# Kernel tuning notes

Measured on AMD Instinct MI355X. Metric: run time of the kernel, lower is better.

## Reference

```python
import jax, jax.numpy as jnp
import numpy as np
from jax import lax

NB_ITERS = 10
HS = 3        # nb_kerhalfsize
HS_LIF = 3    # nb_kerhalfsize_LIF
DN = ('NCDHW', 'OIDHW', 'NCDHW')


def std_kernel(sigma, halfsize):
    # sigma: (C,1,1,1) -> normalized Gaussian kernel (C,1,k,k,k)
    r = jnp.arange(-halfsize, halfsize + 1, dtype=jnp.float32)
    x, y, z = jnp.meshgrid(r, r, r, indexing='ij')  # (k,k,k)
    d2 = x ** 2 + y ** 2 + z ** 2
    sig2 = sigma.reshape(-1, 1, 1, 1) ** 2          # (C,1,1,1)
    ker = jnp.exp(-d2[None] / (2.0 * sig2))         # (C,k,k,k)
    ker = ker / (ker.sum(axis=(1, 2, 3), keepdims=True) + 1e-15)
    return ker[:, None]                              # (C,1,k,k,k)


def dconv(x, ker, halfsize):
    # depthwise (grouped, groups=C) 3D conv with 'same' zero padding
    C = x.shape[1]
    pad = [(halfsize, halfsize)] * 3
    return lax.conv_general_dilated(x, ker, window_strides=(1, 1, 1),
                                    padding=pad, feature_group_count=C,
                                    dimension_numbers=DN)


def setup_inputs() -> dict:
    key = jax.random.key(0)
    k1, k2 = jax.random.split(key)
    C = 4
    shape = (1, C, 96, 96, 96)
    o = jax.random.normal(k1, shape, dtype=jnp.float32)
    I = jax.random.uniform(k2, (1, 1, 96, 96, 96), dtype=jnp.float32)
    sigma2 = jnp.ones((C, 1, 1, 1), dtype=jnp.float32)
    sigma3 = jnp.ones((C, 1, 1, 1), dtype=jnp.float32)
    eta = jnp.ones((1,), dtype=jnp.float32)
    lam = jnp.ones((1,), dtype=jnp.float32) * 5.0
    mu = jnp.ones((1,), dtype=jnp.float32) * 5.0
    return {'o': o, 'I': I, 'sigma2': sigma2, 'sigma3': sigma3,
            'eta': eta, 'lam': lam, 'mu': mu}


def reference(o, I, sigma2, sigma3, eta, lam, mu):
    u = jax.nn.softmax(o / eta, axis=1)
    ker = std_kernel(sigma2, HS)
    ker_lif = std_kernel(sigma3, HS_LIF)
    # conv of the all-ones tensor is loop-invariant (boundary normalization)
    conv_ones = dconv(jnp.ones_like(u), ker_lif, HS_LIF)
    I2 = I ** 2
    for _ in range(NB_ITERS):
        uI = u * I
        C1 = dconv(uI, ker_lif, HS_LIF)
        C2 = dconv(u, ker_lif, HS_LIF)
        Cn = (C1 + 1e-6) / (C2 + 1e-6)
        Lif = (dconv(Cn ** 2, ker_lif, HS_LIF)
               - 2.0 * I * dconv(Cn, ker_lif, HS_LIF)
               + I2 * conv_ones)
        q = dconv(1.0 - 2.0 * u, ker, HS)
        u = jax.nn.softmax((o - mu * Lif - lam * q) / eta, axis=1)
    return u
```

## Files before the change

kernel.cpp:

```cpp
#include <hip/hip_runtime.h>
#include <math.h>

#define PLANE  9216
#define PLANE4 2304
#define VOL    884736
#define VOL4   221184
#define NC     4
#define K      7
#define HSR    3
#define SEGZ   8
#define NSEGZ  12

#define YT     16
#define YTH    22
#define TPBYX  192
#define LINW   100
#define MIDW   108
#define NF4    528

__device__ __forceinline__ float4 f4zero() { return make_float4(0.f, 0.f, 0.f, 0.f); }
__device__ __forceinline__ float4 f4fma(float t, float4 a, float4 s) {
    s.x = fmaf(t, a.x, s.x); s.y = fmaf(t, a.y, s.y);
    s.z = fmaf(t, a.z, s.z); s.w = fmaf(t, a.w, s.w);
    return s;
}
__device__ __forceinline__ float4 f4fmasq(float t, float4 a, float4 s) {
    s.x = fmaf(t, a.x * a.x, s.x); s.y = fmaf(t, a.y * a.y, s.y);
    s.z = fmaf(t, a.z * a.z, s.z); s.w = fmaf(t, a.w * a.w, s.w);
    return s;
}
__device__ __forceinline__ float4 f4mul(float4 a, float4 b) {
    return make_float4(a.x * b.x, a.y * b.y, a.z * b.z, a.w * b.w);
}

__global__ void tables_kernel(const float* __restrict__ sigma2,
                              const float* __restrict__ sigma3,
                              float* __restrict__ taps2, float* __restrict__ taps3,
                              float* __restrict__ B2, float* __restrict__ B3)
{
    int t = threadIdx.x;
    if (t < 2 * NC) {
        int c = t % NC;
        const float* sig = (t < NC) ? sigma2 : sigma3;
        float* taps = (t < NC) ? taps2 : taps3;
        float sv = sig[c];
        float s2 = sv * sv;
        float w[K];
        float sum = 0.f;
        for (int j = 0; j < K; j++) {
            float d = (float)(j - HSR);
            w[j] = expf(-d * d / (2.f * s2));
            sum += w[j];
        }
        float inv = 1.f / sum;
        for (int j = 0; j < K; j++) taps[c * K + j] = w[j] * inv;
    }
    __syncthreads();
    for (int i = t; i < NC * 96; i += blockDim.x) {
        int c = i / 96, p = i % 96;
        float s2v = 0.f, s3v = 0.f;
        for (int j = 0; j < K; j++) {
            int q = p + j - HSR;
            if (q >= 0 && q < 96) { s2v += taps2[c * K + j]; s3v += taps3[c * K + j]; }
        }
        B2[i] = s2v;
        B3[i] = s3v;
    }
}

__global__ __launch_bounds__(256) void softmax0_kernel(const float* __restrict__ o,
                                                       const float* __restrict__ eta,
                                                       float* __restrict__ u)
{
    int i = blockIdx.x * 256 + threadIdx.x;
    const float4* O = (const float4*)o;
    float4* U = (float4*)u;
    float inv_eta = 1.f / eta[0];
    float4 a0 = O[i], a1 = O[i + VOL4], a2 = O[i + 2 * VOL4], a3 = O[i + 3 * VOL4];
#define SM_COMP(f)                                                              \
    {                                                                           \
        float b0 = a0.f * inv_eta, b1 = a1.f * inv_eta;                         \
        float b2 = a2.f * inv_eta, b3 = a3.f * inv_eta;                         \
        float m = fmaxf(fmaxf(b0, b1), fmaxf(b2, b3));                          \
        float e0 = __expf(b0 - m), e1 = __expf(b1 - m);                         \
        float e2 = __expf(b2 - m), e3 = __expf(b3 - m);                         \
        float inv = 1.f / (e0 + e1 + e2 + e3);                                  \
        a0.f = e0 * inv; a1.f = e1 * inv; a2.f = e2 * inv; a3.f = e3 * inv;     \
    }
    SM_COMP(x) SM_COMP(y) SM_COMP(z) SM_COMP(w)
    U[i] = a0; U[i + VOL4] = a1; U[i + 2 * VOL4] = a2; U[i + 3 * VOL4] = a3;
}

__global__ __launch_bounds__(256) void pass1_z(const float* __restrict__ u,
                                               const float* __restrict__ I,
                                               const float* __restrict__ taps2,
                                               const float* __restrict__ taps3,
                                               float* __restrict__ a0, float* __restrict__ a1,
                                               float* __restrict__ a2)
{
    int p4 = blockIdx.x * 256 + threadIdx.x;
    int s  = blockIdx.y;
    int c  = blockIdx.z;
    int z0 = s * SEGZ;
    const float4* ub = (const float4*)(u + (size_t)c * VOL) + p4;
    const float4* Ib = (const float4*)I + p4;
    float t3[K], t2[K];
#pragma unroll
    for (int j = 0; j < K; j++) { t3[j] = taps3[c * K + j]; t2[j] = taps2[c * K + j]; }
    float4 wu[K], wui[K];
#pragma unroll
    for (int j = 0; j < K - 1; j++) {
        int z = z0 + j - HSR;
        float4 uv = f4zero(), iv = f4zero();
        if (z >= 0 && z < 96) { uv = ub[z * PLANE4]; iv = Ib[z * PLANE4]; }
        wu[j] = uv; wui[j] = f4mul(uv, iv);
    }
    float4* o0 = (float4*)(a0 + (size_t)c * VOL) + p4;
    float4* o1 = (float4*)(a1 + (size_t)c * VOL) + p4;
    float4* o2 = (float4*)(a2 + (size_t)c * VOL) + p4;
    for (int k = 0; k < SEGZ; k++) {
        int z = z0 + k, zl = z + HSR;
        float4 uv = f4zero(), iv = f4zero();
        if (zl < 96) { uv = ub[zl * PLANE4]; iv = Ib[zl * PLANE4]; }
        wu[K - 1] = uv; wui[K - 1] = f4mul(uv, iv);
        float4 s0 = f4zero(), s1 = f4zero(), s2 = f4zero();
#pragma unroll
        for (int j = 0; j < K; j++) {
            s0 = f4fma(t3[j], wui[j], s0);
            s1 = f4fma(t3[j], wu[j], s1);
            s2 = f4fma(t2[j], wu[j], s2);
        }
        o0[z * PLANE4] = s0;
        o1[z * PLANE4] = s1;
        o2[z * PLANE4] = s2;
#pragma unroll
        for (int j = 0; j < K - 1; j++) { wu[j] = wu[j + 1]; wui[j] = wui[j + 1]; }
    }
}

__global__ __launch_bounds__(TPBYX) void pass2_yx(const float* __restrict__ a0,
                                                  const float* __restrict__ a1,
                                                  const float* __restrict__ a2,
                                                  const float* __restrict__ taps2,
                                                  const float* __restrict__ taps3,
                                                  const float* __restrict__ B2,
                                                  float* __restrict__ Cn,
                                                  float* __restrict__ q)
{
    __shared__ float lin[3][YTH * LINW];
    __shared__ float mid[3][YT * MIDW];
    int yt = blockIdx.x, z = blockIdx.y, c = blockIdx.z;
    int y0 = yt * YT, tid = threadIdx.x;
    size_t base = (size_t)c * VOL + (size_t)z * PLANE;
    {
        const float4* g0 = (const float4*)(a0 + base);
        const float4* g1 = (const float4*)(a1 + base);
        const float4* g2 = (const float4*)(a2 + base);
#pragma unroll
        for (int i4 = tid; i4 < NF4; i4 += TPBYX) {
            int r = i4 / 24, k = i4 - r * 24;
            int gy = y0 - HSR + r;
            bool ok = (gy >= 0 && gy < 96);
            int gi = gy * 24 + k;
            float4 v0 = ok ? g0[gi] : f4zero();
            float4 v1 = ok ? g1[gi] : f4zero();
            float4 v2 = ok ? g2[gi] : f4zero();
            int li = r * LINW + k * 4;
            *(float4*)&lin[0][li] = v0;
            *(float4*)&lin[1][li] = v1;
            *(float4*)&lin[2][li] = v2;
        }
    }
    if (tid < 128) {
        int r = tid >> 3, p = tid & 7;
        int idx = r * MIDW + (p < 4 ? p : 96 + p);
        mid[0][idx] = 0.f; mid[1][idx] = 0.f; mid[2][idx] = 0.f;
    }
    float t3[K], t2[K];
#pragma unroll
    for (int j = 0; j < K; j++) { t3[j] = taps3[c * K + j]; t2[j] = taps2[c * K + j]; }
    __syncthreads();
    int r  = tid / 12;
    int xb = (tid - r * 12) * 8;
#pragma unroll
    for (int f = 0; f < 3; f++) {
        const float* tp = (f < 2) ? t3 : t2;
        float4 mA = f4zero(), mB = f4zero();
#pragma unroll
        for (int j = 0; j < K; j++) {
            const float4* lp = (const float4*)&lin[f][(r + j) * LINW + xb];
            mA = f4fma(tp[j], lp[0], mA);
            mB = f4fma(tp[j], lp[1], mB);
        }
        float4* mp = (float4*)&mid[f][r * MIDW + 4 + xb];
        mp[0] = mA; mp[1] = mB;
    }
    __syncthreads();
    float outA[8], outB[8], outC[8];
    {
        float wf[16];
#pragma unroll
        for (int f = 0; f < 3; f++) {
            const float* tp = (f < 2) ? t3 : t2;
            const float4* wp = (const float4*)&mid[f][r * MIDW + xb];
            *(float4*)&wf[0]  = wp[0];
            *(float4*)&wf[4]  = wp[1];
            *(float4*)&wf[8]  = wp[2];
            *(float4*)&wf[12] = wp[3];
            float* dst = (f == 0) ? outA : (f == 1) ? outB : outC;
#pragma unroll
            for (int k = 0; k < 8; k++) {
                float s = 0.f;
#pragma unroll
                for (int j = 0; j < K; j++) s = fmaf(tp[j], wf[k + j + 1], s);
                dst[k] = s;
            }
        }
    }
    int y = y0 + r;
    float Bz = B2[c * 96 + z];
    float By = B2[c * 96 + y];
    float Bx[8];
    {
        const float4* bx = (const float4*)&B2[c * 96 + xb];
        *(float4*)&Bx[0] = bx[0];
        *(float4*)&Bx[4] = bx[1];
    }
    float co[8], qo[8];
#pragma unroll
    for (int k = 0; k < 8; k++) {
        co[k] = (outA[k] + 1e-6f) / (outB[k] + 1e-6f);
        qo[k] = fmaf(Bz * By, Bx[k], -2.f * outC[k]);
    }
    float* cp = Cn + base + y * 96 + xb;
    float* qp = q  + base + y * 96 + xb;
    *(float4*)cp       = *(float4*)&co[0];
    *(float4*)(cp + 4) = *(float4*)&co[4];
    *(float4*)qp       = *(float4*)&qo[0];
    *(float4*)(qp + 4) = *(float4*)&qo[4];
}

__global__ __launch_bounds__(256) void pass4_z(const float* __restrict__ Cn,
                                               const float* __restrict__ taps3,
                                               float* __restrict__ b0, float* __restrict__ b1)
{
    int p4 = blockIdx.x * 256 + threadIdx.x;
    int s  = blockIdx.y;
    int c  = blockIdx.z;
    int z0 = s * SEGZ;
    const float4* ib = (const float4*)(Cn + (size_t)c * VOL) + p4;
    float t3[K];
#pragma unroll
    for (int j = 0; j < K; j++) t3[j] = taps3[c * K + j];
    float4 w[K];
#pragma unroll
    for (int j = 0; j < K - 1; j++) {
        int z = z0 + j - HSR;
        float4 v = f4zero();
        if (z >= 0 && z < 96) v = ib[z * PLANE4];
        w[j] = v;
    }
    float4* o0 = (float4*)(b0 + (size_t)c * VOL) + p4;
    float4* o1 = (float4*)(b1 + (size_t)c * VOL) + p4;
    for (int k = 0; k < SEGZ; k++) {
        int z = z0 + k, zl = z + HSR;
        float4 v = f4zero();
        if (zl < 96) v = ib[zl * PLANE4];
        w[K - 1] = v;
        float4 s0 = f4zero(), s1 = f4zero();
#pragma unroll
        for (int j = 0; j < K; j++) {
            s0 = f4fma(t3[j], w[j], s0);
            s1 = f4fmasq(t3[j], w[j], s1);
        }
        o0[z * PLANE4] = s0;
        o1[z * PLANE4] = s1;
#pragma unroll
        for (int j = 0; j < K - 1; j++) w[j] = w[j + 1];
    }
}

__global__ __launch_bounds__(TPBYX) void pass5_yx(const float* __restrict__ cz0,
                                                  const float* __restrict__ cz1,
                                                  const float* __restrict__ q,
                                                  const float* __restrict__ o,
                                                  const float* __restrict__ I,
                                                  const float* __restrict__ taps3,
                                                  const float* __restrict__ B3,
                                                  const float* __restrict__ eta,
                                                  const float* __restrict__ lam,
                                                  const float* __restrict__ mu,
                                                  float* __restrict__ argb)
{
    __shared__ float lin[2][YTH * LINW];
    __shared__ float mid[2][YT * MIDW];
    int yt = blockIdx.x, z = blockIdx.y, c = blockIdx.z;
    int y0 = yt * YT, tid = threadIdx.x;
    size_t base = (size_t)c * VOL + (size_t)z * PLANE;
    {
        const float4* g0 = (const float4*)(cz0 + base);
        const float4* g1 = (const float4*)(cz1 + base);
#pragma unroll
        for (int i4 = tid; i4 < NF4; i4 += TPBYX) {
            int r = i4 / 24, k = i4 - r * 24;
            int gy = y0 - HSR + r;
            bool ok = (gy >= 0 && gy < 96);
            int gi = gy * 24 + k;
            float4 v0 = ok ? g0[gi] : f4zero();
            float4 v1 = ok ? g1[gi] : f4zero();
            int li = r * LINW + k * 4;
            *(float4*)&lin[0][li] = v0;
            *(float4*)&lin[1][li] = v1;
        }
    }
    if (tid < 128) {
        int r = tid >> 3, p = tid & 7;
        int idx = r * MIDW + (p < 4 ? p : 96 + p);
        mid[0][idx] = 0.f; mid[1][idx] = 0.f;
    }
    float t3[K];
#pragma unroll
    for (int j = 0; j < K; j++) t3[j] = taps3[c * K + j];
    __syncthreads();
    int r  = tid / 12;
    int xb = (tid - r * 12) * 8;
#pragma unroll
    for (int f = 0; f < 2; f++) {
        float4 mA = f4zero(), mB = f4zero();
#pragma unroll
        for (int j = 0; j < K; j++) {
            const float4* lp = (const float4*)&lin[f][(r + j) * LINW + xb];
            mA = f4fma(t3[j], lp[0], mA);
            mB = f4fma(t3[j], lp[1], mB);
        }
        float4* mp = (float4*)&mid[f][r * MIDW + 4 + xb];
        mp[0] = mA; mp[1] = mB;
    }
    __syncthreads();
    float d0[8], d1[8];
    {
        float wf[16];
#pragma unroll
        for (int f = 0; f < 2; f++) {
            const float4* wp = (const float4*)&mid[f][r * MIDW + xb];
            *(float4*)&wf[0]  = wp[0];
            *(float4*)&wf[4]  = wp[1];
            *(float4*)&wf[8]  = wp[2];
            *(float4*)&wf[12] = wp[3];
            float* dst = (f == 0) ? d0 : d1;
#pragma unroll
            for (int k = 0; k < 8; k++) {
                float s = 0.f;
#pragma unroll
                for (int j = 0; j < K; j++) s = fmaf(t3[j], wf[k + j + 1], s);
                dst[k] = s;
            }
        }
    }
    int y = y0 + r;
    int v = z * PLANE + y * 96 + xb;
    float inv_eta = 1.f / eta[0];
    float lamv = lam[0], muv = mu[0];
    float Bz = B3[c * 96 + z];
    float By = B3[c * 96 + y];
    float Bx[8], Ivv[8], ov[8], qv[8];
    {
        const float4* bx = (const float4*)&B3[c * 96 + xb];
        *(float4*)&Bx[0] = bx[0]; *(float4*)&Bx[4] = bx[1];
        const float4* ip = (const float4*)&I[v];
        *(float4*)&Ivv[0] = ip[0]; *(float4*)&Ivv[4] = ip[1];
        const float4* op = (const float4*)&o[(size_t)c * VOL + v];
        *(float4*)&ov[0] = op[0]; *(float4*)&ov[4] = op[1];
        const float4* qp = (const float4*)&q[(size_t)c * VOL + v];
        *(float4*)&qv[0] = qp[0]; *(float4*)&qv[4] = qp[1];
    }
    float res[8];
#pragma unroll
    for (int k = 0; k < 8; k++) {
        float Iv = Ivv[k];
        float cones = Bz * By * Bx[k];
        float Lif = d1[k] - 2.f * Iv * d0[k] + Iv * Iv * cones;
        res[k] = (ov[k] - muv * Lif - lamv * qv[k]) * inv_eta;
    }
    float* ap = argb + base + y * 96 + xb;
    *(float4*)ap       = *(float4*)&res[0];
    *(float4*)(ap + 4) = *(float4*)&res[4];
}

__global__ __launch_bounds__(256) void pass6_softmax(const float* __restrict__ argb,
                                                     float* __restrict__ u)
{
    int i = blockIdx.x * 256 + threadIdx.x;
    const float4* A = (const float4*)argb;
    float4* U = (float4*)u;
    float4 a0 = A[i], a1 = A[i + VOL4], a2 = A[i + 2 * VOL4], a3 = A[i + 3 * VOL4];
#define SM2_COMP(f)                                                             \
    {                                                                           \
        float m = fmaxf(fmaxf(a0.f, a1.f), fmaxf(a2.f, a3.f));                  \
        float e0 = __expf(a0.f - m), e1 = __expf(a1.f - m);                     \
        float e2 = __expf(a2.f - m), e3 = __expf(a3.f - m);                     \
        float inv = 1.f / (e0 + e1 + e2 + e3);                                  \
        a0.f = e0 * inv; a1.f = e1 * inv; a2.f = e2 * inv; a3.f = e3 * inv;     \
    }
    SM2_COMP(x) SM2_COMP(y) SM2_COMP(z) SM2_COMP(w)
    U[i] = a0; U[i + VOL4] = a1; U[i + 2 * VOL4] = a2; U[i + 3 * VOL4] = a3;
}

extern "C" void kernel_launch(void* const* d_in, const int* in_sizes, int n_in,
                              void* d_out, int out_size, void* d_ws, size_t ws_size,
                              hipStream_t stream)
{
    const float* o      = (const float*)d_in[0];
    const float* I      = (const float*)d_in[1];
    const float* sigma2 = (const float*)d_in[2];
    const float* sigma3 = (const float*)d_in[3];
    const float* eta    = (const float*)d_in[4];
    const float* lam    = (const float*)d_in[5];
    const float* mu     = (const float*)d_in[6];
    float* u = (float*)d_out;

    float* wsf = (float*)d_ws;
    float* taps2 = wsf;
    float* taps3 = wsf + 32;
    float* B2    = wsf + 64;
    float* B3    = wsf + 64 + NC * 96;
    float* buf   = wsf + 1024;
    const size_t VCs = (size_t)NC * VOL;
    float* a0 = buf;
    float* a1 = buf + VCs;
    float* a2 = buf + 2 * VCs;
    float* Cn = buf + 3 * VCs;
    float* qb = buf + 4 * VCs;
    float* c0 = buf + 5 * VCs;
    float* c1 = buf + 6 * VCs;

    const dim3 gridZ(PLANE4 / 256, NSEGZ, NC);
    const dim3 gridYX(96 / YT, 96, NC);
    const int gridV4 = VOL4 / 256;

    tables_kernel<<<1, 512, 0, stream>>>(sigma2, sigma3, taps2, taps3, B2, B3);
    softmax0_kernel<<<gridV4, 256, 0, stream>>>(o, eta, u);
    for (int it = 0; it < 10; it++) {
        pass1_z<<<gridZ, 256, 0, stream>>>(u, I, taps2, taps3, a0, a1, a2);
        pass2_yx<<<gridYX, TPBYX, 0, stream>>>(a0, a1, a2, taps2, taps3, B2, Cn, qb);
        pass4_z<<<gridZ, 256, 0, stream>>>(Cn, taps3, c0, c1);
        pass5_yx<<<gridYX, TPBYX, 0, stream>>>(c0, c1, qb, o, I, taps3, B3,
                                               eta, lam, mu, a0);
        pass6_softmax<<<gridV4, 256, 0, stream>>>(a0, u);
    }
}
```

Measured before the change: 704.6 us.

## Fuse softmax into z-pass and drop separate softmax kernel per iteration

Each iteration's softmax is now folded into the first z-direction conv pass: pass1 reads the raw logits for all four channels, computes the softmax on the fly for each plane it loads, and convolves. The softmax kernel and the write and read of u are gone from the loop, and the final softmax runs once at the end. This trades a full-volume read and write per iteration for recomputing the softmax on every plane load, about 7x redundant exp work, with fewer threads (64 per block, 2 floats each). pass4 also gets retuned block and segment sizes, and pass5 now writes its logits into the Cn buffer.

After: 728.6 us. +3.4%, slower.

```diff
diff --git a/kernel.cpp b/kernel.cpp
--- a/kernel.cpp
+++ b/kernel.cpp
@@ -2,14 +2,18 @@
 #include <math.h>
 
 #define PLANE  9216
+#define PLANE2 4608
 #define PLANE4 2304
 #define VOL    884736
+#define VOL2   442368
 #define VOL4   221184
 #define NC     4
 #define K      7
 #define HSR    3
 #define SEGZ   8
 #define NSEGZ  12
+#define SEGZ4  16
+#define NSEGZ4 6
 
 #define YT     16
 #define YTH    22
@@ -29,8 +33,10 @@
     s.z = fmaf(t, a.z * a.z, s.z); s.w = fmaf(t, a.w * a.w, s.w);
     return s;
 }
-__device__ __forceinline__ float4 f4mul(float4 a, float4 b) {
-    return make_float4(a.x * b.x, a.y * b.y, a.z * b.z, a.w * b.w);
+__device__ __forceinline__ float2 f2zero() { return make_float2(0.f, 0.f); }
+__device__ __forceinline__ float2 f2fma(float t, float2 a, float2 s) {
+    s.x = fmaf(t, a.x, s.x); s.y = fmaf(t, a.y, s.y);
+    return s;
 }
 
 __global__ void tables_kernel(const float* __restrict__ sigma2,
@@ -91,51 +97,93 @@
     U[i] = a0; U[i + VOL4] = a1; U[i + 2 * VOL4] = a2; U[i + 3 * VOL4] = a3;
 }
 
-__global__ __launch_bounds__(256) void pass1_z(const float* __restrict__ u,
-                                               const float* __restrict__ I,
-                                               const float* __restrict__ taps2,
-                                               const float* __restrict__ taps3,
-                                               float* __restrict__ a0, float* __restrict__ a1,
-                                               float* __restrict__ a2)
-{
-    int p4 = blockIdx.x * 256 + threadIdx.x;
-    int s  = blockIdx.y;
-    int c  = blockIdx.z;
-    int z0 = s * SEGZ;
-    const float4* ub = (const float4*)(u + (size_t)c * VOL) + p4;
-    const float4* Ib = (const float4*)I + p4;
-    float t3[K], t2[K];
-#pragma unroll
-    for (int j = 0; j < K; j++) { t3[j] = taps3[c * K + j]; t2[j] = taps2[c * K + j]; }
-    float4 wu[K], wui[K];
-#pragma unroll
-    for (int j = 0; j < K - 1; j++) {
-        int z = z0 + j - HSR;
-        float4 uv = f4zero(), iv = f4zero();
-        if (z >= 0 && z < 96) { uv = ub[z * PLANE4]; iv = Ib[z * PLANE4]; }
-        wu[j] = uv; wui[j] = f4mul(uv, iv);
-    }
-    float4* o0 = (float4*)(a0 + (size_t)c * VOL) + p4;
-    float4* o1 = (float4*)(a1 + (size_t)c * VOL) + p4;
-    float4* o2 = (float4*)(a2 + (size_t)c * VOL) + p4;
+__global__ __launch_bounds__(64) void pass1f(const float* __restrict__ araw,
+                                             const float* __restrict__ I,
+                                             const float* __restrict__ taps2,
+                                             const float* __restrict__ taps3,
+                                             const float* __restrict__ eta,
+                                             float* __restrict__ a0, float* __restrict__ a1,
+                                             float* __restrict__ a2)
+{
+    int p2 = blockIdx.x * 64 + threadIdx.x;
+    int z0 = blockIdx.y * SEGZ;
+    float inv_eta = 1.f / eta[0];
+    float t3[NC][K], t2[NC][K];
+#pragma unroll
+    for (int c = 0; c < NC; c++)
+#pragma unroll
+        for (int j = 0; j < K; j++) { t3[c][j] = taps3[c * K + j]; t2[c][j] = taps2[c * K + j]; }
+    const float2* A  = (const float2*)araw;
+    const float2* Ip = (const float2*)I;
+    float2 uw[NC][K];
+    float2 iw[K];
+
+#define LOADPLANE(zz, dst_j)                                                     \
+    {                                                                            \
+        int z_ = (zz);                                                           \
+        if (z_ >= 0 && z_ < 96) {                                                \
+            int off = z_ * PLANE2 + p2;                                          \
+            float2 q0 = A[off];                                                  \
+            float2 q1 = A[off + VOL2];                                           \
+            float2 q2 = A[off + 2 * VOL2];                                       \
+            float2 q3 = A[off + 3 * VOL2];                                       \
+            iw[dst_j] = Ip[off];                                                 \
+            float b0, b1, b2, b3, m_, e0, e1, e2, e3, inv_;                      \
+            b0 = q0.x * inv_eta; b1 = q1.x * inv_eta;                            \
+            b2 = q2.x * inv_eta; b3 = q3.x * inv_eta;                            \
+            m_ = fmaxf(fmaxf(b0, b1), fmaxf(b2, b3));                            \
+            e0 = __expf(b0 - m_); e1 = __expf(b1 - m_);                          \
+            e2 = __expf(b2 - m_); e3 = __expf(b3 - m_);                          \
+            inv_ = 1.f / (e0 + e1 + e2 + e3);                                    \
+            uw[0][dst_j].x = e0 * inv_; uw[1][dst_j].x = e1 * inv_;              \
+            uw[2][dst_j].x = e2 * inv_; uw[3][dst_j].x = e3 * inv_;              \
+            b0 = q0.y * inv_eta; b1 = q1.y * inv_eta;                            \
+            b2 = q2.y * inv_eta; b3 = q3.y * inv_eta;                            \
+            m_ = fmaxf(fmaxf(b0, b1), fmaxf(b2, b3));                            \
+            e0 = __expf(b0 - m_); e1 = __expf(b1 - m_);                          \
+            e2 = __expf(b2 - m_); e3 = __expf(b3 - m_);                          \
+            inv_ = 1.f / (e0 + e1 + e2 + e3);                                    \
+            uw[0][dst_j].y = e0 * inv_; uw[1][dst_j].y = e1 * inv_;              \
+            uw[2][dst_j].y = e2 * inv_; uw[3][dst_j].y = e3 * inv_;              \
+        } else {                                                                 \
+            iw[dst_j] = f2zero();                                                \
+            uw[0][dst_j] = f2zero(); uw[1][dst_j] = f2zero();                    \
+            uw[2][dst_j] = f2zero(); uw[3][dst_j] = f2zero();                    \
+        }                                                                        \
+    }
+
+#pragma unroll
+    for (int j = 0; j < K - 1; j++) LOADPLANE(z0 + j - HSR, j)
+
+    float2* O0 = (float2*)a0;
+    float2* O1 = (float2*)a1;
+    float2* O2 = (float2*)a2;
     for (int k = 0; k < SEGZ; k++) {
-        int z = z0 + k, zl = z + HSR;
-        float4 uv = f4zero(), iv = f4zero();
-        if (zl < 96) { uv = ub[zl * PLANE4]; iv = Ib[zl * PLANE4]; }
-        wu[K - 1] = uv; wui[K - 1] = f4mul(uv, iv);
-        float4 s0 = f4zero(), s1 = f4zero(), s2 = f4zero();
-#pragma unroll
-        for (int j = 0; j < K; j++) {
-            s0 = f4fma(t3[j], wui[j], s0);
-            s1 = f4fma(t3[j], wu[j], s1);
-            s2 = f4fma(t2[j], wu[j], s2);
-        }
-        o0[z * PLANE4] = s0;
-        o1[z * PLANE4] = s1;
-        o2[z * PLANE4] = s2;
-#pragma unroll
-        for (int j = 0; j < K - 1; j++) { wu[j] = wu[j + 1]; wui[j] = wui[j + 1]; }
-    }
+        LOADPLANE(z0 + k + HSR, K - 1)
+        int ob = (z0 + k) * PLANE2 + p2;
+#pragma unroll
+        for (int c = 0; c < NC; c++) {
+            float2 s0 = f2zero(), s1 = f2zero(), s2 = f2zero();
+#pragma unroll
+            for (int j = 0; j < K; j++) {
+                float2 uv = uw[c][j];
+                float2 ui = make_float2(uv.x * iw[j].x, uv.y * iw[j].y);
+                s0 = f2fma(t3[c][j], ui, s0);
+                s1 = f2fma(t3[c][j], uv, s1);
+                s2 = f2fma(t2[c][j], uv, s2);
+            }
+            O0[c * VOL2 + ob] = s0;
+            O1[c * VOL2 + ob] = s1;
+            O2[c * VOL2 + ob] = s2;
+        }
+#pragma unroll
+        for (int j = 0; j < K - 1; j++) {
+            iw[j] = iw[j + 1];
+#pragma unroll
+            for (int c = 0; c < NC; c++) uw[c][j] = uw[c][j + 1];
+        }
+    }
+#undef LOADPLANE
 }
 
 __global__ __launch_bounds__(TPBYX) void pass2_yx(const float* __restrict__ a0,
@@ -240,14 +288,14 @@
     *(float4*)(qp + 4) = *(float4*)&qo[4];
 }
 
-__global__ __launch_bounds__(256) void pass4_z(const float* __restrict__ Cn,
+__global__ __launch_bounds__(128) void pass4_z(const float* __restrict__ Cn,
                                                const float* __restrict__ taps3,
                                                float* __restrict__ b0, float* __restrict__ b1)
 {
-    int p4 = blockIdx.x * 256 + threadIdx.x;
+    int p4 = blockIdx.x * 128 + threadIdx.x;
     int s  = blockIdx.y;
     int c  = blockIdx.z;
-    int z0 = s * SEGZ;
+    int z0 = s * SEGZ4;
     const float4* ib = (const float4*)(Cn + (size_t)c * VOL) + p4;
     float t3[K];
 #pragma unroll
@@ -262,7 +310,7 @@
     }
     float4* o0 = (float4*)(b0 + (size_t)c * VOL) + p4;
     float4* o1 = (float4*)(b1 + (size_t)c * VOL) + p4;
-    for (int k = 0; k < SEGZ; k++) {
+    for (int k = 0; k < SEGZ4; k++) {
         int z = z0 + k, zl = z + HSR;
         float4 v = f4zero();
         if (zl < 96) v = ib[zl * PLANE4];
@@ -287,7 +335,6 @@
                                                   const float* __restrict__ I,
                                                   const float* __restrict__ taps3,
                                                   const float* __restrict__ B3,
-                                                  const float* __restrict__ eta,
                                                   const float* __restrict__ lam,
                                                   const float* __restrict__ mu,
                                                   float* __restrict__ argb)
@@ -359,7 +406,6 @@
     }
     int y = y0 + r;
     int v = z * PLANE + y * 96 + xb;
-    float inv_eta = 1.f / eta[0];
     float lamv = lam[0], muv = mu[0];
     float Bz = B3[c * 96 + z];
     float By = B3[c * 96 + y];
@@ -380,30 +426,11 @@
         float Iv = Ivv[k];
         float cones = Bz * By * Bx[k];
         float Lif = d1[k] - 2.f * Iv * d0[k] + Iv * Iv * cones;
-        res[k] = (ov[k] - muv * Lif - lamv * qv[k]) * inv_eta;
+        res[k] = ov[k] - muv * Lif - lamv * qv[k];
     }
     float* ap = argb + base + y * 96 + xb;
     *(float4*)ap       = *(float4*)&res[0];
     *(float4*)(ap + 4) = *(float4*)&res[4];
-}
-
-__global__ __launch_bounds__(256) void pass6_softmax(const float* __restrict__ argb,
-                                                     float* __restrict__ u)
-{
-    int i = blockIdx.x * 256 + threadIdx.x;
-    const float4* A = (const float4*)argb;
-    float4* U = (float4*)u;
-    float4 a0 = A[i], a1 = A[i + VOL4], a2 = A[i + 2 * VOL4], a3 = A[i + 3 * VOL4];
-#define SM2_COMP(f)                                                             \
-    {                                                                           \
-        float m = fmaxf(fmaxf(a0.f, a1.f), fmaxf(a2.f, a3.f));                  \
-        float e0 = __expf(a0.f - m), e1 = __expf(a1.f - m);                     \
-        float e2 = __expf(a2.f - m), e3 = __expf(a3.f - m);                     \
-        float inv = 1.f / (e0 + e1 + e2 + e3);                                  \
-        a0.f = e0 * inv; a1.f = e1 * inv; a2.f = e2 * inv; a3.f = e3 * inv;     \
-    }
-    SM2_COMP(x) SM2_COMP(y) SM2_COMP(z) SM2_COMP(w)
-    U[i] = a0; U[i + VOL4] = a1; U[i + 2 * VOL4] = a2; U[i + 3 * VOL4] = a3;
 }
 
 extern "C" void kernel_launch(void* const* d_in, const int* in_sizes, int n_in,
@@ -434,18 +461,19 @@
     float* c0 = buf + 5 * VCs;
     float* c1 = buf + 6 * VCs;
 
-    const dim3 gridZ(PLANE4 / 256, NSEGZ, NC);
+    const dim3 grid1(PLANE2 / 64, NSEGZ);
     const dim3 gridYX(96 / YT, 96, NC);
+    const dim3 grid4(PLANE4 / 128, NSEGZ4, NC);
     const int gridV4 = VOL4 / 256;
 
     tables_kernel<<<1, 512, 0, stream>>>(sigma2, sigma3, taps2, taps3, B2, B3);
-    softmax0_kernel<<<gridV4, 256, 0, stream>>>(o, eta, u);
     for (int it = 0; it < 10; it++) {
-        pass1_z<<<gridZ, 256, 0, stream>>>(u, I, taps2, taps3, a0, a1, a2);
+        const float* argin = (it == 0) ? o : Cn;
+        pass1f<<<grid1, 64, 0, stream>>>(argin, I, taps2, taps3, eta, a0, a1, a2);
         pass2_yx<<<gridYX, TPBYX, 0, stream>>>(a0, a1, a2, taps2, taps3, B2, Cn, qb);
-        pass4_z<<<gridZ, 256, 0, stream>>>(Cn, taps3, c0, c1);
+        pass4_z<<<grid4, 128, 0, stream>>>(Cn, taps3, c0, c1);
         pass5_yx<<<gridYX, TPBYX, 0, stream>>>(c0, c1, qb, o, I, taps3, B3,
-                                               eta, lam, mu, a0);
-        pass6_softmax<<<gridV4, 256, 0, stream>>>(a0, u);
-    }
-}
+                                               lam, mu, Cn);
+    }
+    softmax0_kernel<<<gridV4, 256, 0, stream>>>(Cn, eta, u);
+}
```

## Move q yx-convolution into pass5 and reuse eta-scaling softmax kernel

Applied to the files above, without the earlier changes.

The yx smoothing of the q field (a2) moves from pass2 into pass5, so the intermediate q buffer is no longer written and read back each iteration. pass2 now handles only the two LIF fields, and pass5 handles three. The separate final softmax kernel is replaced by the initial softmax kernel, which applies 1/eta itself, so pass5 drops its eta multiply. pass4_z also switches to 128-thread blocks with 16-slice z segments, giving more blocks with less halo reload. The cost is heavier shared-memory use and register pressure in pass5.

Result: no change. 714.9 us (+1.5%).

```diff
diff --git a/kernel.cpp b/kernel.cpp
--- a/kernel.cpp
+++ b/kernel.cpp
@@ -10,6 +10,8 @@
 #define HSR    3
 #define SEGZ   8
 #define NSEGZ  12
+#define SEGZ4  16
+#define NSEGZ4 6
 
 #define YT     16
 #define YTH    22
@@ -68,15 +70,15 @@
     }
 }
 
-__global__ __launch_bounds__(256) void softmax0_kernel(const float* __restrict__ o,
-                                                       const float* __restrict__ eta,
-                                                       float* __restrict__ u)
+__global__ __launch_bounds__(256) void softmax_kernel(const float* __restrict__ a,
+                                                      const float* __restrict__ eta,
+                                                      float* __restrict__ u)
 {
     int i = blockIdx.x * 256 + threadIdx.x;
-    const float4* O = (const float4*)o;
+    const float4* A = (const float4*)a;
     float4* U = (float4*)u;
     float inv_eta = 1.f / eta[0];
-    float4 a0 = O[i], a1 = O[i + VOL4], a2 = O[i + 2 * VOL4], a3 = O[i + 3 * VOL4];
+    float4 a0 = A[i], a1 = A[i + VOL4], a2 = A[i + 2 * VOL4], a3 = A[i + 3 * VOL4];
 #define SM_COMP(f)                                                              \
     {                                                                           \
         float b0 = a0.f * inv_eta, b1 = a1.f * inv_eta;                         \
@@ -140,12 +142,137 @@
 
 __global__ __launch_bounds__(TPBYX) void pass2_yx(const float* __restrict__ a0,
                                                   const float* __restrict__ a1,
+                                                  const float* __restrict__ taps3,
+                                                  float* __restrict__ Cn)
+{
+    __shared__ float lin[2][YTH * LINW];
+    __shared__ float mid[2][YT * MIDW];
+    int yt = blockIdx.x, z = blockIdx.y, c = blockIdx.z;
+    int y0 = yt * YT, tid = threadIdx.x;
+    size_t base = (size_t)c * VOL + (size_t)z * PLANE;
+    {
+        const float4* g0 = (const float4*)(a0 + base);
+        const float4* g1 = (const float4*)(a1 + base);
+#pragma unroll
+        for (int i4 = tid; i4 < NF4; i4 += TPBYX) {
+            int r = i4 / 24, k = i4 - r * 24;
+            int gy = y0 - HSR + r;
+            bool ok = (gy >= 0 && gy < 96);
+            int gi = gy * 24 + k;
+            float4 v0 = ok ? g0[gi] : f4zero();
+            float4 v1 = ok ? g1[gi] : f4zero();
+            int li = r * LINW + k * 4;
+            *(float4*)&lin[0][li] = v0;
+            *(float4*)&lin[1][li] = v1;
+        }
+    }
+    if (tid < 128) {
+        int r = tid >> 3, p = tid & 7;
+        int idx = r * MIDW + (p < 4 ? p : 96 + p);
+        mid[0][idx] = 0.f; mid[1][idx] = 0.f;
+    }
+    float t3[K];
+#pragma unroll
+    for (int j = 0; j < K; j++) t3[j] = taps3[c * K + j];
+    __syncthreads();
+    int r  = tid / 12;
+    int xb = (tid - r * 12) * 8;
+#pragma unroll
+    for (int f = 0; f < 2; f++) {
+        float4 mA = f4zero(), mB = f4zero();
+#pragma unroll
+        for (int j = 0; j < K; j++) {
+            const float4* lp = (const float4*)&lin[f][(r + j) * LINW + xb];
+            mA = f4fma(t3[j], lp[0], mA);
+            mB = f4fma(t3[j], lp[1], mB);
+        }
+        float4* mp = (float4*)&mid[f][r * MIDW + 4 + xb];
+        mp[0] = mA; mp[1] = mB;
+    }
+    __syncthreads();
+    float outA[8], outB[8];
+    {
+        float wf[16];
+#pragma unroll
+        for (int f = 0; f < 2; f++) {
+            const float4* wp = (const float4*)&mid[f][r * MIDW + xb];
+            *(float4*)&wf[0]  = wp[0];
+            *(float4*)&wf[4]  = wp[1];
+            *(float4*)&wf[8]  = wp[2];
+            *(float4*)&wf[12] = wp[3];
+            float* dst = (f == 0) ? outA : outB;
+#pragma unroll
+            for (int k = 0; k < 8; k++) {
+                float s = 0.f;
+#pragma unroll
+                for (int j = 0; j < K; j++) s = fmaf(t3[j], wf[k + j + 1], s);
+                dst[k] = s;
+            }
+        }
+    }
+    int y = y0 + r;
+    float co[8];
+#pragma unroll
+    for (int k = 0; k < 8; k++)
+        co[k] = (outA[k] + 1e-6f) / (outB[k] + 1e-6f);
+    float* cp = Cn + base + y * 96 + xb;
+    *(float4*)cp       = *(float4*)&co[0];
+    *(float4*)(cp + 4) = *(float4*)&co[4];
+}
+
+__global__ __launch_bounds__(128) void pass4_z(const float* __restrict__ Cn,
+                                               const float* __restrict__ taps3,
+                                               float* __restrict__ b0, float* __restrict__ b1)
+{
+    int p4 = blockIdx.x * 128 + threadIdx.x;
+    int s  = blockIdx.y;
+    int c  = blockIdx.z;
+    int z0 = s * SEGZ4;
+    const float4* ib = (const float4*)(Cn + (size_t)c * VOL) + p4;
+    float t3[K];
+#pragma unroll
+    for (int j = 0; j < K; j++) t3[j] = taps3[c * K + j];
+    float4 w[K];
+#pragma unroll
+    for (int j = 0; j < K - 1; j++) {
+        int z = z0 + j - HSR;
+        float4 v = f4zero();
+        if (z >= 0 && z < 96) v = ib[z * PLANE4];
+        w[j] = v;
+    }
+    float4* o0 = (float4*)(b0 + (size_t)c * VOL) + p4;
+    float4* o1 = (float4*)(b1 + (size_t)c * VOL) + p4;
+    for (int k = 0; k < SEGZ4; k++) {
+        int z = z0 + k, zl = z + HSR;
+        float4 v = f4zero();
+        if (zl < 96) v = ib[zl * PLANE4];
+        w[K - 1] = v;
+        float4 s0 = f4zero(), s1 = f4zero();
+#pragma unroll
+        for (int j = 0; j < K; j++) {
+            s0 = f4fma(t3[j], w[j], s0);
+            s1 = f4fmasq(t3[j], w[j], s1);
+        }
+        o0[z * PLANE4] = s0;
+        o1[z * PLANE4] = s1;
+#pragma unroll
+        for (int j = 0; j < K - 1; j++) w[j] = w[j + 1];
+    }
+}
+
+__global__ __launch_bounds__(TPBYX) void pass5_yx(const float* __restrict__ cz0,
+                                                  const float* __restrict__ cz1,
                                                   const float* __restrict__ a2,
+                                                  const float* __restrict__ o,
+                                                  const float* __restrict__ I,
                                                   const float* __restrict__ taps2,
                                                   const float* __restrict__ taps3,
                                                   const float* __restrict__ B2,
-                                                  float* __restrict__ Cn,
-                                                  float* __restrict__ q)
+                                                  const float* __restrict__ B3,
+                                                  const float* __restrict__ eta,
+                                                  const float* __restrict__ lam,
+                                                  const float* __restrict__ mu,
+                                                  float* __restrict__ argb)
 {
     __shared__ float lin[3][YTH * LINW];
     __shared__ float mid[3][YT * MIDW];
@@ -153,8 +280,8 @@
     int y0 = yt * YT, tid = threadIdx.x;
     size_t base = (size_t)c * VOL + (size_t)z * PLANE;
     {
-        const float4* g0 = (const float4*)(a0 + base);
-        const float4* g1 = (const float4*)(a1 + base);
+        const float4* g0 = (const float4*)(cz0 + base);
+        const float4* g1 = (const float4*)(cz1 + base);
         const float4* g2 = (const float4*)(a2 + base);
 #pragma unroll
         for (int i4 = tid; i4 < NF4; i4 += TPBYX) {
@@ -196,7 +323,7 @@
         mp[0] = mA; mp[1] = mB;
     }
     __syncthreads();
-    float outA[8], outB[8], outC[8];
+    float d0[8], d1[8], s2[8];
     {
         float wf[16];
 #pragma unroll
@@ -207,152 +334,12 @@
             *(float4*)&wf[4]  = wp[1];
             *(float4*)&wf[8]  = wp[2];
             *(float4*)&wf[12] = wp[3];
-            float* dst = (f == 0) ? outA : (f == 1) ? outB : outC;
+            float* dst = (f == 0) ? d0 : (f == 1) ? d1 : s2;
 #pragma unroll
             for (int k = 0; k < 8; k++) {
                 float s = 0.f;
 #pragma unroll
                 for (int j = 0; j < K; j++) s = fmaf(tp[j], wf[k + j + 1], s);
-                dst[k] = s;
-            }
-        }
-    }
-    int y = y0 + r;
-    float Bz = B2[c * 96 + z];
-    float By = B2[c * 96 + y];
-    float Bx[8];
-    {
-        const float4* bx = (const float4*)&B2[c * 96 + xb];
-        *(float4*)&Bx[0] = bx[0];
-        *(float4*)&Bx[4] = bx[1];
-    }
-    float co[8], qo[8];
-#pragma unroll
-    for (int k = 0; k < 8; k++) {
-        co[k] = (outA[k] + 1e-6f) / (outB[k] + 1e-6f);
-        qo[k] = fmaf(Bz * By, Bx[k], -2.f * outC[k]);
-    }
-    float* cp = Cn + base + y * 96 + xb;
-    float* qp = q  + base + y * 96 + xb;
-    *(float4*)cp       = *(float4*)&co[0];
-    *(float4*)(cp + 4) = *(float4*)&co[4];
-    *(float4*)qp       = *(float4*)&qo[0];
-    *(float4*)(qp + 4) = *(float4*)&qo[4];
-}
-
-__global__ __launch_bounds__(256) void pass4_z(const float* __restrict__ Cn,
-                                               const float* __restrict__ taps3,
-                                               float* __restrict__ b0, float* __restrict__ b1)
-{
-    int p4 = blockIdx.x * 256 + threadIdx.x;
-    int s  = blockIdx.y;
-    int c  = blockIdx.z;
-    int z0 = s * SEGZ;
-    const float4* ib = (const float4*)(Cn + (size_t)c * VOL) + p4;
-    float t3[K];
-#pragma unroll
-    for (int j = 0; j < K; j++) t3[j] = taps3[c * K + j];
-    float4 w[K];
-#pragma unroll
-    for (int j = 0; j < K - 1; j++) {
-        int z = z0 + j - HSR;
-        float4 v = f4zero();
-        if (z >= 0 && z < 96) v = ib[z * PLANE4];
-        w[j] = v;
-    }
-    float4* o0 = (float4*)(b0 + (size_t)c * VOL) + p4;
-    float4* o1 = (float4*)(b1 + (size_t)c * VOL) + p4;
-    for (int k = 0; k < SEGZ; k++) {
-        int z = z0 + k, zl = z + HSR;
-        float4 v = f4zero();
-        if (zl < 96) v = ib[zl * PLANE4];
-        w[K - 1] = v;
-        float4 s0 = f4zero(), s1 = f4zero();
-#pragma unroll
-        for (int j = 0; j < K; j++) {
-            s0 = f4fma(t3[j], w[j], s0);
-            s1 = f4fmasq(t3[j], w[j], s1);
-        }
-        o0[z * PLANE4] = s0;
-        o1[z * PLANE4] = s1;
-#pragma unroll
-        for (int j = 0; j < K - 1; j++) w[j] = w[j + 1];
-    }
-}
-
-__global__ __launch_bounds__(TPBYX) void pass5_yx(const float* __restrict__ cz0,
-                                                  const float* __restrict__ cz1,
-                                                  const float* __restrict__ q,
-                                                  const float* __restrict__ o,
-                                                  const float* __restrict__ I,
-                                                  const float* __restrict__ taps3,
-                                                  const float* __restrict__ B3,
-                                                  const float* __restrict__ eta,
-                                                  const float* __restrict__ lam,
-                                                  const float* __restrict__ mu,
-                                                  float* __restrict__ argb)
-{
-    __shared__ float lin[2][YTH * LINW];
-    __shared__ float mid[2][YT * MIDW];
-    int yt = blockIdx.x, z = blockIdx.y, c = blockIdx.z;
-    int y0 = yt * YT, tid = threadIdx.x;
-    size_t base = (size_t)c * VOL + (size_t)z * PLANE;
-    {
-        const float4* g0 = (const float4*)(cz0 + base);
-        const float4* g1 = (const float4*)(cz1 + base);
-#pragma unroll
-        for (int i4 = tid; i4 < NF4; i4 += TPBYX) {
-            int r = i4 / 24, k = i4 - r * 24;
-            int gy = y0 - HSR + r;
-            bool ok = (gy >= 0 && gy < 96);
-            int gi = gy * 24 + k;
-            float4 v0 = ok ? g0[gi] : f4zero();
-            float4 v1 = ok ? g1[gi] : f4zero();
-            int li = r * LINW + k * 4;
-            *(float4*)&lin[0][li] = v0;
-            *(float4*)&lin[1][li] = v1;
-        }
-    }
-    if (tid < 128) {
-        int r = tid >> 3, p = tid & 7;
-        int idx = r * MIDW + (p < 4 ? p : 96 + p);
-        mid[0][idx] = 0.f; mid[1][idx] = 0.f;
-    }
-    float t3[K];
-#pragma unroll
-    for (int j = 0; j < K; j++) t3[j] = taps3[c * K + j];
-    __syncthreads();
-    int r  = tid / 12;
-    int xb = (tid - r * 12) * 8;
-#pragma unroll
-    for (int f = 0; f < 2; f++) {
-        float4 mA = f4zero(), mB = f4zero();
-#pragma unroll
-        for (int j = 0; j < K; j++) {
-            const float4* lp = (const float4*)&lin[f][(r + j) * LINW + xb];
-            mA = f4fma(t3[j], lp[0], mA);
-            mB = f4fma(t3[j], lp[1], mB);
-        }
-        float4* mp = (float4*)&mid[f][r * MIDW + 4 + xb];
-        mp[0] = mA; mp[1] = mB;
-    }
-    __syncthreads();
-    float d0[8], d1[8];
-    {
-        float wf[16];
-#pragma unroll
-        for (int f = 0; f < 2; f++) {
-            const float4* wp = (const float4*)&mid[f][r * MIDW + xb];
-            *(float4*)&wf[0]  = wp[0];
-            *(float4*)&wf[4]  = wp[1];
-            *(float4*)&wf[8]  = wp[2];
-            *(float4*)&wf[12] = wp[3];
-            float* dst = (f == 0) ? d0 : d1;
-#pragma unroll
-            for (int k = 0; k < 8; k++) {
-                float s = 0.f;
-#pragma unroll
-                for (int j = 0; j < K; j++) s = fmaf(t3[j], wf[k + j + 1], s);
                 dst[k] = s;
             }
         }
@@ -361,49 +348,31 @@
     int v = z * PLANE + y * 96 + xb;
     float inv_eta = 1.f / eta[0];
     float lamv = lam[0], muv = mu[0];
-    float Bz = B3[c * 96 + z];
-    float By = B3[c * 96 + y];
-    float Bx[8], Ivv[8], ov[8], qv[8];
+    float Bz3 = B3[c * 96 + z], By3 = B3[c * 96 + y];
+    float Bz2 = B2[c * 96 + z], By2 = B2[c * 96 + y];
+    float Bx3[8], Bx2[8], Ivv[8], ov[8];
     {
-        const float4* bx = (const float4*)&B3[c * 96 + xb];
-        *(float4*)&Bx[0] = bx[0]; *(float4*)&Bx[4] = bx[1];
+        const float4* bx3 = (const float4*)&B3[c * 96 + xb];
+        *(float4*)&Bx3[0] = bx3[0]; *(float4*)&Bx3[4] = bx3[1];
+        const float4* bx2 = (const float4*)&B2[c * 96 + xb];
+        *(float4*)&Bx2[0] = bx2[0]; *(float4*)&Bx2[4] = bx2[1];
         const float4* ip = (const float4*)&I[v];
         *(float4*)&Ivv[0] = ip[0]; *(float4*)&Ivv[4] = ip[1];
         const float4* op = (const float4*)&o[(size_t)c * VOL + v];
         *(float4*)&ov[0] = op[0]; *(float4*)&ov[4] = op[1];
-        const float4* qp = (const float4*)&q[(size_t)c * VOL + v];
-        *(float4*)&qv[0] = qp[0]; *(float4*)&qv[4] = qp[1];
     }
     float res[8];
 #pragma unroll
     for (int k = 0; k < 8; k++) {
         float Iv = Ivv[k];
-        float cones = Bz * By * Bx[k];
+        float cones = Bz3 * By3 * Bx3[k];
         float Lif = d1[k] - 2.f * Iv * d0[k] + Iv * Iv * cones;
-        res[k] = (ov[k] - muv * Lif - lamv * qv[k]) * inv_eta;
+        float qv  = fmaf(Bz2 * By2, Bx2[k], -2.f * s2[k]);
+        res[k] = ov[k] - muv * Lif - lamv * qv;
     }
     float* ap = argb + base + y * 96 + xb;
     *(float4*)ap       = *(float4*)&res[0];
     *(float4*)(ap + 4) = *(float4*)&res[4];
-}
-
-__global__ __launch_bounds__(256) void pass6_softmax(const float* __restrict__ argb,
-                                                     float* __restrict__ u)
-{
-    int i = blockIdx.x * 256 + threadIdx.x;
-    const float4* A = (const float4*)argb;
-    float4* U = (float4*)u;
-    float4 a0 = A[i], a1 = A[i + VOL4], a2 = A[i + 2 * VOL4], a3 = A[i + 3 * VOL4];
-#define SM2_COMP(f)                                                             \
-    {                                                                           \
-        float m = fmaxf(fmaxf(a0.f, a1.f), fmaxf(a2.f, a3.f));                  \
-        float e0 = __expf(a0.f - m), e1 = __expf(a1.f - m);                     \
-        float e2 = __expf(a2.f - m), e3 = __expf(a3.f - m);                     \
-        float inv = 1.f / (e0 + e1 + e2 + e3);                                  \
-        a0.f = e0 * inv; a1.f = e1 * inv; a2.f = e2 * inv; a3.f = e3 * inv;     \
-    }
-    SM2_COMP(x) SM2_COMP(y) SM2_COMP(z) SM2_COMP(w)
-    U[i] = a0; U[i + VOL4] = a1; U[i + 2 * VOL4] = a2; U[i + 3 * VOL4] = a3;
 }
 
 extern "C" void kernel_launch(void* const* d_in, const int* in_sizes, int n_in,
@@ -430,22 +399,22 @@
     float* a1 = buf + VCs;
     float* a2 = buf + 2 * VCs;
     float* Cn = buf + 3 * VCs;
-    float* qb = buf + 4 * VCs;
-    float* c0 = buf + 5 * VCs;
-    float* c1 = buf + 6 * VCs;
-
-    const dim3 gridZ(PLANE4 / 256, NSEGZ, NC);
+    float* c0 = buf + 4 * VCs;
+    float* c1 = buf + 5 * VCs;
+
+    const dim3 grid1(PLANE4 / 256, NSEGZ, NC);
     const dim3 gridYX(96 / YT, 96, NC);
+    const dim3 grid4(PLANE4 / 128, NSEGZ4, NC);
     const int gridV4 = VOL4 / 256;
 
     tables_kernel<<<1, 512, 0, stream>>>(sigma2, sigma3, taps2, taps3, B2, B3);
-    softmax0_kernel<<<gridV4, 256, 0, stream>>>(o, eta, u);
+    softmax_kernel<<<gridV4, 256, 0, stream>>>(o, eta, u);
     for (int it = 0; it < 10; it++) {
-        pass1_z<<<gridZ, 256, 0, stream>>>(u, I, taps2, taps3, a0, a1, a2);
-        pass2_yx<<<gridYX, TPBYX, 0, stream>>>(a0, a1, a2, taps2, taps3, B2, Cn, qb);
-        pass4_z<<<gridZ, 256, 0, stream>>>(Cn, taps3, c0, c1);
-        pass5_yx<<<gridYX, TPBYX, 0, stream>>>(c0, c1, qb, o, I, taps3, B3,
-                                               eta, lam, mu, a0);
-        pass6_softmax<<<gridV4, 256, 0, stream>>>(a0, u);
-    }
-}
+        pass1_z<<<grid1, 256, 0, stream>>>(u, I, taps2, taps3, a0, a1, a2);
+        pass2_yx<<<gridYX, TPBYX, 0, stream>>>(a0, a1, taps3, Cn);
+        pass4_z<<<grid4, 128, 0, stream>>>(Cn, taps3, c0, c1);
+        pass5_yx<<<gridYX, TPBYX, 0, stream>>>(c0, c1, a2, o, I, taps2, taps3,
+                                               B2, B3, eta, lam, mu, a0);
+        softmax_kernel<<<gridV4, 256, 0, stream>>>(a0, eta, u);
+    }
+}
```
